# Kernel tuning notes

Measured on AMD Instinct MI355X. Metric: run time of the kernel, lower is better.

## Reference

```python
import jax, jax.numpy as jnp
import numpy as np

B, L, DIM, HEAD_DIM, COND = 16, 1025, 1024, 64, 256
N_HEADS = DIM // HEAD_DIM
EPS = 1e-6


def _make_cos_sin():
    # freqs: head_dim//8 log-spaced frequencies in [pi, 10*pi]
    freqs = np.exp(np.linspace(np.log(np.pi), np.log(10 * np.pi), HEAD_DIM // 8)).astype(np.float32)
    # axial positions on a 32x32 grid (cell centers in [-1, 1]), with a zero pos prepended
    g = np.linspace(-1.0, 1.0, 33, dtype=np.float32)
    g = (g[:-1] + g[1:]) / 2
    hh, ww = np.meshgrid(g, g, indexing='ij')
    pos = np.stack([hh.ravel(), ww.ravel()], axis=-1)          # [1024, 2]
    pos = np.concatenate([np.zeros((1, 2), np.float32), pos])  # [1025, 2]
    theta = np.concatenate([pos[:, 0:1] * freqs, pos[:, 1:2] * freqs], axis=-1)  # [L, head_dim//4]
    return jnp.asarray(np.cos(theta)), jnp.asarray(np.sin(theta))


def setup_inputs() -> dict:
    key = jax.random.key(0)
    kx, kc, kn, kq, ko = jax.random.split(key, 5)
    cos, sin = _make_cos_sin()
    return {
        'x': jax.random.normal(kx, (B, L, DIM), jnp.float32),
        'cond': jax.random.normal(kc, (B, COND), jnp.float32),
        'w_norm': jax.random.normal(kn, (DIM, COND), jnp.float32) * 0.02,   # AdaRMSNorm linear (zero-init in training; random here)
        'w_qkv': jax.random.normal(kq, (3 * DIM, DIM), jnp.float32) * 0.02,
        'w_out': jax.random.normal(ko, (DIM, DIM), jnp.float32) * 0.02,
        'cos': cos,  # [L, head_dim//4]
        'sin': sin,
    }


def _rope(t, cos, sin):
    # partial non-interleaved rotary: rotate first 2*cos.shape[-1] dims, leave the rest
    half = cos.shape[-1]                      # head_dim//4
    t1 = t[..., :half]
    t2 = t[..., half:2 * half]
    rest = t[..., 2 * half:]
    c = cos[None, :, None, :]                 # [1, L, 1, half]
    s = sin[None, :, None, :]
    return jnp.concatenate([t1 * c - t2 * s, t2 * c + t1 * s, rest], axis=-1)


def reference(x, cond, w_norm, w_qkv, w_out, cos, sin):
    skip = x
    # AdaRMSNorm: scale = cond-linear + 1, normalized by rms(x) in fp32
    scale = cond @ w_norm.T + 1.0                                    # [B, D]
    mean_sq = jnp.mean(jnp.square(x.astype(jnp.float32)), axis=-1, keepdims=True)
    xn = x * (scale[:, None, :] * jax.lax.rsqrt(mean_sq + EPS)).astype(x.dtype)
    # QKV projection
    qkv = (xn @ w_qkv.T).reshape(B, L, 3, N_HEADS, HEAD_DIM)
    q, k, v = qkv[:, :, 0], qkv[:, :, 1], qkv[:, :, 2]               # [B, L, H, hd]
    q = _rope(q, cos, sin)
    k = _rope(k, cos, sin)
    # causal attention (flash_attn default softmax scale = head_dim**-0.5)
    sm_scale = 1.0 / jnp.sqrt(jnp.asarray(HEAD_DIM, jnp.float32))
    scores = jnp.einsum('blhd,bmhd->bhlm', q, k) * sm_scale
    causal = jnp.tril(jnp.ones((L, L), bool))
    scores = jnp.where(causal[None, None], scores, jnp.finfo(scores.dtype).min)
    attn = jax.nn.softmax(scores, axis=-1)
    o = jnp.einsum('bhlm,bmhd->blhd', attn, v).reshape(B, L, DIM)
    return o @ w_out.T + skip
```

## Files before the change

kernel.cpp:

```cpp
#include <hip/hip_runtime.h>
#include <hip/hip_bf16.h>
#include <cstdint>

typedef __bf16 bf16;
typedef bf16 bf16x4 __attribute__((ext_vector_type(4)));
typedef bf16 bf16x8 __attribute__((ext_vector_type(8)));
typedef float f32x4 __attribute__((ext_vector_type(4)));
typedef float f32x16 __attribute__((ext_vector_type(16)));
typedef uint32_t u32x4 __attribute__((ext_vector_type(4)));

#define NB 16
#define NL 1025
#define NDIM 1024
#define NHEADS 16
#define NCOND 256
#define NBH (NB*NHEADS)
#define NML (NB*NL)
#define LP 1056
#define NSLOT 17
#define QSCALE (0.125f * 1.44269504088896340736f)

__device__ __forceinline__ void gload16(const void* g, void* l) {
  __builtin_amdgcn_global_load_lds(
      (const __attribute__((address_space(1))) void*)(uintptr_t)g,
      (__attribute__((address_space(3))) void*)(uintptr_t)l,
      16, 0, 0);
}

__device__ __forceinline__ float fexp2(float x) {
  return __builtin_amdgcn_exp2f(x);
}

__device__ __forceinline__ uint32_t cvtpk(float lo, float hi) {
  uint32_t r;
  asm("v_cvt_pk_bf16_f32 %0, %1, %2" : "=v"(r) : "v"(lo), "v"(hi));
  return r;
}

__device__ __forceinline__ f32x16 zero16() {
  f32x16 z;
#pragma unroll
  for (int i = 0; i < 16; ++i) z[i] = 0.f;
  return z;
}

__global__ __launch_bounds__(256) void k_scale(const float* __restrict__ cond,
                                               const float* __restrict__ wn,
                                               float* __restrict__ scl) {
  __shared__ float cs[NCOND];
  const int b = blockIdx.x, t = threadIdx.x;
  cs[t] = cond[b * NCOND + t];
  __syncthreads();
#pragma unroll
  for (int dd = 0; dd < 4; ++dd) {
    const int d = t * 4 + dd;
    const float4* w = (const float4*)(wn + (size_t)d * NCOND);
    float acc = 1.0f;
    for (int c4 = 0; c4 < NCOND / 4; ++c4) {
      float4 wv = w[c4];
      acc += wv.x * cs[c4*4] + wv.y * cs[c4*4+1] + wv.z * cs[c4*4+2] + wv.w * cs[c4*4+3];
    }
    scl[b * NDIM + d] = acc;
  }
}

__global__ __launch_bounds__(256) void k_cast(const float* __restrict__ src,
                                              bf16* __restrict__ dst, int n) {
  const int i = (blockIdx.x * 256 + threadIdx.x) * 4;
  if (i < n) {
    float4 v = *(const float4*)(src + i);
    bf16x4 o;
    o[0] = (bf16)v.x; o[1] = (bf16)v.y; o[2] = (bf16)v.z; o[3] = (bf16)v.w;
    *(bf16x4*)(dst + i) = o;
  }
}

__global__ __launch_bounds__(256) void k_rmsnorm(const float* __restrict__ x,
                                                 const float* __restrict__ scl,
                                                 bf16* __restrict__ xn) {
  const int row = blockIdx.x, t = threadIdx.x;
  const int b = row / NL;
  const float* xr = x + (size_t)row * NDIM;
  float4 v = *(const float4*)(xr + t * 4);
  float ss = v.x*v.x + v.y*v.y + v.z*v.z + v.w*v.w;
#pragma unroll
  for (int o = 1; o < 64; o <<= 1) ss += __shfl_xor(ss, o);
  __shared__ float red[4];
  if ((t & 63) == 0) red[t >> 6] = ss;
  __syncthreads();
  const float tot = red[0] + red[1] + red[2] + red[3];
  const float rn = rsqrtf(tot * (1.0f / NDIM) + 1e-6f);
  const float4 sc = *(const float4*)(scl + b * NDIM + t * 4);
  bf16x4 o4;
  o4[0] = (bf16)(v.x * sc.x * rn);
  o4[1] = (bf16)(v.y * sc.y * rn);
  o4[2] = (bf16)(v.z * sc.z * rn);
  o4[3] = (bf16)(v.w * sc.w * rn);
  *(bf16x4*)(xn + (size_t)row * NDIM + t * 4) = o4;
}

template <int EPI>
__global__ __launch_bounds__(256) void k_gemm(const bf16* __restrict__ A,
                                              const bf16* __restrict__ Bm,
                                              int M, int N, int K,
                                              float* __restrict__ Cf,
                                              const float* __restrict__ skip,
                                              bf16* __restrict__ qro,
                                              bf16* __restrict__ kro,
                                              bf16* __restrict__ vto,
                                              const float* __restrict__ cosT,
                                              const float* __restrict__ sinT) {
  __shared__ bf16 Als[2][128 * 64];
  __shared__ bf16 Bls[2][128 * 64];
  const int t = threadIdx.x;
  const int wave = t >> 6, lane = t & 63;
  const int g = lane >> 4, c = lane & 15;
  const int wm = wave >> 1, wn_ = wave & 1;

  const int nxb = N >> 7;
  const int nwg = gridDim.x;
  const int cpx = nwg >> 3;
  const int bid = blockIdx.x;
  const int swz = (nwg & 7) ? bid : (bid & 7) * cpx + (bid >> 3);
  const int m0 = (swz / nxb) * 128, n0 = (swz % nxb) * 128;
  const int NT = K >> 6;

  const int srow = lane >> 3;
  const int scol = ((lane & 7) ^ srow) * 8;

  f32x4 acc[4][4];
#pragma unroll
  for (int i = 0; i < 4; ++i)
#pragma unroll
    for (int j = 0; j < 4; ++j) acc[i][j] = f32x4{0.f, 0.f, 0.f, 0.f};

  auto stage = [&](int kt, int q) {
    const int k0 = kt << 6;
#pragma unroll
    for (int i = 0; i < 4; ++i) {
      const int seg = wave * 4 + i;
      int arow = m0 + seg * 8 + srow;
      if (arow >= M) arow = M - 1;
      gload16(A + (size_t)arow * K + k0 + scol, &Als[q][seg * 512]);
      const int brow = n0 + seg * 8 + srow;
      gload16(Bm + (size_t)brow * K + k0 + scol, &Bls[q][seg * 512]);
    }
  };

  stage(0, 0);
  for (int kt = 0; kt < NT; ++kt) {
    const int cur = kt & 1;
    if (kt + 1 < NT) {
      stage(kt + 1, cur ^ 1);
      asm volatile("s_waitcnt vmcnt(8)" ::: "memory");
    } else {
      asm volatile("s_waitcnt vmcnt(0)" ::: "memory");
    }
    __builtin_amdgcn_s_barrier();
    asm volatile("" ::: "memory");
#pragma unroll
    for (int kc = 0; kc < 2; ++kc) {
      bf16x8 af[4], bfr[4];
#pragma unroll
      for (int mi = 0; mi < 4; ++mi) {
        const int r = wm * 64 + mi * 16 + c;
        const int gg = ((kc * 4 + g) ^ (c & 7)) * 8;
        af[mi] = *(const bf16x8*)&Als[cur][r * 64 + gg];
      }
#pragma unroll
      for (int ni = 0; ni < 4; ++ni) {
        const int r = wn_ * 64 + ni * 16 + c;
        const int gg = ((kc * 4 + g) ^ (c & 7)) * 8;
        bfr[ni] = *(const bf16x8*)&Bls[cur][r * 64 + gg];
      }
      __builtin_amdgcn_s_setprio(1);
#pragma unroll
      for (int mi = 0; mi < 4; ++mi)
#pragma unroll
        for (int ni = 0; ni < 4; ++ni)
          acc[mi][ni] = __builtin_amdgcn_mfma_f32_16x16x32_bf16(af[mi], bfr[ni], acc[mi][ni], 0, 0, 0);
      __builtin_amdgcn_s_setprio(0);
    }
    asm volatile("" ::: "memory");
    __builtin_amdgcn_s_barrier();
  }

  if (EPI == 1) {
#pragma unroll
    for (int mi = 0; mi < 4; ++mi) {
      const int rb = m0 + wm * 64 + mi * 16 + g * 4;
#pragma unroll
      for (int ni = 0; ni < 4; ++ni) {
        const int col = n0 + wn_ * 64 + ni * 16 + c;
#pragma unroll
        for (int j = 0; j < 4; ++j) {
          const int row = rb + j;
          if (row < M) {
            const size_t idx = (size_t)row * N + col;
            Cf[idx] = acc[mi][ni][j] + skip[idx];
          }
        }
      }
    }
  } else {
    const int ncol0 = n0 + wn_ * 64;
    const int type = ncol0 >> 10;
    const int hd = (ncol0 & 1023) >> 6;
    if (type == 2) {
#pragma unroll
      for (int mi = 0; mi < 4; ++mi) {
        const int rb = m0 + wm * 64 + mi * 16 + g * 4;
        const int b0 = rb / NL, b3 = (rb + 3) / NL;
        if (rb + 3 < M && b0 == b3) {
          const int l0_ = rb - b0 * NL;
          const size_t bhb = (size_t)(b0 * NHEADS + hd) * 64;
#pragma unroll
          for (int ni = 0; ni < 4; ++ni) {
            const int d = ni * 16 + c;
            bf16x4 v4;
#pragma unroll
            for (int j = 0; j < 4; ++j) v4[j] = (bf16)acc[mi][ni][j];
            *(bf16x4*)(vto + (bhb + d) * LP + l0_) = v4;
          }
        } else {
#pragma unroll
          for (int j = 0; j < 4; ++j) {
            const int row = rb + j;
            if (row < M) {
              const int b_ = row / NL, l = row - b_ * NL;
              const size_t bhb = (size_t)(b_ * NHEADS + hd) * 64;
#pragma unroll
              for (int ni = 0; ni < 4; ++ni)
                vto[(bhb + ni * 16 + c) * LP + l] = (bf16)acc[mi][ni][j];
            }
          }
        }
      }
    } else {
      bf16* dst = (type == 0) ? qro : kro;
      const float qs = (type == 0) ? QSCALE : 1.0f;
#pragma unroll
      for (int mi = 0; mi < 4; ++mi) {
        const int rb = m0 + wm * 64 + mi * 16 + g * 4;
#pragma unroll
        for (int j = 0; j < 4; ++j) {
          const int row = rb + j;
          if (row < M) {
            const int b_ = row / NL, l = row - b_ * NL;
            const float cf = cosT[l * 16 + c], sf = sinT[l * 16 + c];
            const float a0 = acc[mi][0][j], a1 = acc[mi][1][j];
            const float r0 = (a0 * cf - a1 * sf) * qs;
            const float r1 = (a1 * cf + a0 * sf) * qs;
            const float r2 = acc[mi][2][j] * qs;
            const float r3 = acc[mi][3][j] * qs;
            const size_t bse = ((size_t)(b_ * NHEADS + hd) * NL + l) * 64;
            dst[bse + c]      = (bf16)r0;
            dst[bse + 16 + c] = (bf16)r1;
            dst[bse + 32 + c] = (bf16)r2;
            dst[bse + 48 + c] = (bf16)r3;
          }
        }
      }
    }
  }
}

__global__ __launch_bounds__(64) void k_attn(const bf16* __restrict__ qr,
                                             const bf16* __restrict__ kr,
                                             const bf16* __restrict__ vt,
                                             bf16* __restrict__ oa) {
  const int bid = blockIdx.x;
  const int lbid = (bid & 7) * (NBH * NSLOT / 8) + (bid >> 3);
  const int slot = lbid % NSLOT, bh = lbid / NSLOT;
  const int b = bh >> 4, h = bh & 15;
  const int lane = threadIdx.x;
  const int ql = lane & 31;
  const int hh = lane >> 5;
  const bf16* qb = qr + (size_t)bh * NL * 64;
  const bf16* kb = kr + (size_t)bh * NL * 64;
  const bf16* vb = vt + (size_t)bh * 64 * LP;

  auto run = [&](const int t) {
    const int q0 = t * 32;
    const int qabs = q0 + ql;
    const int qrow = (q0 + ql < NL) ? q0 + ql : NL - 1;
    bf16x8 bQ[4];
#pragma unroll
    for (int kc = 0; kc < 4; ++kc)
      bQ[kc] = *(const bf16x8*)(qb + (size_t)qrow * 64 + kc * 16 + hh * 8);

    f32x16 od0 = zero16(), od1 = zero16();
    float ls = 0.f;

    const int qmax = (q0 + 31 < NL - 1) ? q0 + 31 : NL - 1;
    const int nt = qmax / 64 + 1;

    bf16x8 aK[2][4];
    auto loadK = [&](int kv0) {
#pragma unroll
      for (int blk = 0; blk < 2; ++blk) {
        int r = kv0 + blk * 32 + ql; if (r >= NL) r = NL - 1;
        const bf16* kp = kb + (size_t)r * 64 + hh * 8;
#pragma unroll
        for (int kc = 0; kc < 4; ++kc)
          aK[blk][kc] = *(const bf16x8*)(kp + kc * 16);
      }
    };
    loadK(0);

    for (int tk = 0; tk < nt; ++tk) {
      const int kv0 = tk * 64;

      bf16x8 vf[2][4];
#pragma unroll
      for (int dblk = 0; dblk < 2; ++dblk) {
        const bf16* vp = vb + (size_t)(dblk * 32 + ql) * LP;
#pragma unroll
        for (int kc = 0; kc < 4; ++kc) {
          int col = kv0 + kc * 16 + hh * 8;
          if (col > LP - 8) col = LP - 8;
          vf[dblk][kc] = *(const bf16x8*)(vp + col);
        }
      }

      f32x16 s0 = zero16(), s1 = zero16();
#pragma unroll
      for (int kc = 0; kc < 4; ++kc)
        s0 = __builtin_amdgcn_mfma_f32_32x32x16_bf16(aK[0][kc], bQ[kc], s0, 0, 0, 0);
#pragma unroll
      for (int kc = 0; kc < 4; ++kc)
        s1 = __builtin_amdgcn_mfma_f32_32x32x16_bf16(aK[1][kc], bQ[kc], s1, 0, 0, 0);

      if (tk + 1 < nt) loadK(kv0 + 64);

      const bool needmask = (kv0 + 63 > q0);
      bf16x8 pa[4];
#pragma unroll
      for (int blk = 0; blk < 2; ++blk) {
        const f32x16& s = blk ? s1 : s0;
        float p[16];
#pragma unroll
        for (int r = 0; r < 16; ++r) {
          float v = s[r];
          if (needmask) {
            const int kvabs = kv0 + blk * 32 + (r & 3) + 8 * (r >> 2) + 4 * hh;
            if (kvabs > qabs) v = -1e30f;
          }
          p[r] = fexp2(v);
        }
        ls += (((p[0]+p[1])+(p[2]+p[3])) + ((p[4]+p[5])+(p[6]+p[7])))
            + (((p[8]+p[9])+(p[10]+p[11])) + ((p[12]+p[13])+(p[14]+p[15])));
        uint32_t w[8];
#pragma unroll
        for (int a = 0; a < 8; ++a) w[a] = cvtpk(p[2*a], p[2*a+1]);
        const uint32_t sel0 = hh ? w[0] : w[2];
        const uint32_t sel1 = hh ? w[1] : w[3];
        const uint32_t sel2 = hh ? w[4] : w[6];
        const uint32_t sel3 = hh ? w[5] : w[7];
        const uint32_t ex0 = (uint32_t)__shfl_xor((int)sel0, 32);
        const uint32_t ex1 = (uint32_t)__shfl_xor((int)sel1, 32);
        const uint32_t ex2 = (uint32_t)__shfl_xor((int)sel2, 32);
        const uint32_t ex3 = (uint32_t)__shfl_xor((int)sel3, 32);
        u32x4 w0_, w1_;
        w0_[0] = hh ? ex0 : w[0];
        w0_[1] = hh ? ex1 : w[1];
        w0_[2] = hh ? w[2] : ex0;
        w0_[3] = hh ? w[3] : ex1;
        w1_[0] = hh ? ex2 : w[4];
        w1_[1] = hh ? ex3 : w[5];
        w1_[2] = hh ? w[6] : ex2;
        w1_[3] = hh ? w[7] : ex3;
        pa[2*blk]     = __builtin_bit_cast(bf16x8, w0_);
        pa[2*blk + 1] = __builtin_bit_cast(bf16x8, w1_);
      }

#pragma unroll
      for (int kc = 0; kc < 4; ++kc) {
        od0 = __builtin_amdgcn_mfma_f32_32x32x16_bf16(pa[kc], vf[0][kc], od0, 0, 0, 0);
        od1 = __builtin_amdgcn_mfma_f32_32x32x16_bf16(pa[kc], vf[1][kc], od1, 0, 0, 0);
      }
    }

    const float tot = ls + __shfl_xor(ls, 32);
    const float invOwn = 1.0f / tot;
#pragma unroll
    for (int r = 0; r < 16; ++r) {
      const int qrl = (r & 3) + 8 * (r >> 2) + 4 * hh;
      const float inv = __shfl(invOwn, qrl);
      const int row = q0 + qrl;
      if (row < NL) {
        const size_t ob = (size_t)(b * NL + row) * NDIM + h * 64;
        oa[ob + ql]      = (bf16)(od0[r] * inv);
        oa[ob + 32 + ql] = (bf16)(od1[r] * inv);
      }
    }
  };

  if (slot < 16) { run(slot); run(31 - slot); }
  else           { run(32); }
}

extern "C" void kernel_launch(void* const* d_in, const int* in_sizes, int n_in,
                              void* d_out, int out_size, void* d_ws, size_t ws_size,
                              hipStream_t stream) {
  const float* x     = (const float*)d_in[0];
  const float* cond  = (const float*)d_in[1];
  const float* wnorm = (const float*)d_in[2];
  const float* wqkv  = (const float*)d_in[3];
  const float* wout  = (const float*)d_in[4];
  const float* cosT  = (const float*)d_in[5];
  const float* sinT  = (const float*)d_in[6];
  float* out = (float*)d_out;
  char* ws = (char*)d_ws;

  float* s_scl = (float*)(ws);
  bf16*  s_wq  = (bf16*)(ws + 65536);
  bf16*  s_wo  = (bf16*)(ws + 6356992);
  bf16*  s_xn  = (bf16*)(ws + 8454144);
  bf16*  s_qr  = (bf16*)(ws + 142802944);
  bf16*  s_kr  = (bf16*)(ws + 176390144);
  bf16*  s_vt  = (bf16*)(ws + 209977344);

  k_scale<<<NB, 256, 0, stream>>>(cond, wnorm, s_scl);
  k_cast<<<3072, 256, 0, stream>>>(wqkv, s_wq, 3 * NDIM * NDIM);
  k_cast<<<1024, 256, 0, stream>>>(wout, s_wo, NDIM * NDIM);
  k_rmsnorm<<<NML, 256, 0, stream>>>(x, s_scl, s_xn);
  k_gemm<2><<<3096, 256, 0, stream>>>(s_xn, s_wq, NML, 3 * NDIM, NDIM,
                                      nullptr, nullptr, s_qr, s_kr, s_vt,
                                      cosT, sinT);
  k_attn<<<NBH * NSLOT, 64, 0, stream>>>(s_qr, s_kr, s_vt, s_xn);
  k_gemm<1><<<1032, 256, 0, stream>>>(s_xn, s_wo, NML, NDIM, NDIM,
                                      out, x, nullptr, nullptr, nullptr,
                                      nullptr, nullptr);
}
```

Measured before the change: 434.0 us.

## Fuse paired query tiles into one KV loop sharing K/V loads

The attention block used to process its two query tiles one after the other, reloading K and V for each. It now walks the KV sequence once and feeds each K/V tile to both query tiles, so the shorter tile A shares loads with tile B. This halves K/V global traffic for paired slots and interleaves independent MFMA/softmax chains to hide latency. In exchange it doubles live accumulators and query registers, which may raise register pressure and lower occupancy.

```diff
diff --git a/kernel.cpp b/kernel.cpp
--- a/kernel.cpp
+++ b/kernel.cpp
@@ -280,107 +280,145 @@
   const bf16* kb = kr + (size_t)bh * NL * 64;
   const bf16* vb = vt + (size_t)bh * 64 * LP;
 
-  auto run = [&](const int t) {
-    const int q0 = t * 32;
-    const int qabs = q0 + ql;
-    const int qrow = (q0 + ql < NL) ? q0 + ql : NL - 1;
-    bf16x8 bQ[4];
+  const int tA = (slot < 16) ? slot : -1;
+  const int tB = (slot < 16) ? 31 - slot : 32;
+  const bool hasA = (tA >= 0);
+
+  const int q0A = tA * 32, q0B = tB * 32;
+  const int qabsA = q0A + ql, qabsB = q0B + ql;
+
+  bf16x8 bQA[4], bQB[4];
+  {
+    const int qrB = (q0B + ql < NL) ? q0B + ql : NL - 1;
 #pragma unroll
     for (int kc = 0; kc < 4; ++kc)
-      bQ[kc] = *(const bf16x8*)(qb + (size_t)qrow * 64 + kc * 16 + hh * 8);
-
-    f32x16 od0 = zero16(), od1 = zero16();
-    float ls = 0.f;
-
-    const int qmax = (q0 + 31 < NL - 1) ? q0 + 31 : NL - 1;
-    const int nt = qmax / 64 + 1;
-
-    bf16x8 aK[2][4];
-    auto loadK = [&](int kv0) {
-#pragma unroll
-      for (int blk = 0; blk < 2; ++blk) {
-        int r = kv0 + blk * 32 + ql; if (r >= NL) r = NL - 1;
-        const bf16* kp = kb + (size_t)r * 64 + hh * 8;
-#pragma unroll
-        for (int kc = 0; kc < 4; ++kc)
-          aK[blk][kc] = *(const bf16x8*)(kp + kc * 16);
-      }
-    };
-    loadK(0);
-
-    for (int tk = 0; tk < nt; ++tk) {
-      const int kv0 = tk * 64;
-
-      bf16x8 vf[2][4];
-#pragma unroll
-      for (int dblk = 0; dblk < 2; ++dblk) {
-        const bf16* vp = vb + (size_t)(dblk * 32 + ql) * LP;
-#pragma unroll
-        for (int kc = 0; kc < 4; ++kc) {
-          int col = kv0 + kc * 16 + hh * 8;
-          if (col > LP - 8) col = LP - 8;
-          vf[dblk][kc] = *(const bf16x8*)(vp + col);
+      bQB[kc] = *(const bf16x8*)(qb + (size_t)qrB * 64 + kc * 16 + hh * 8);
+    const int qrA = hasA ? q0A + ql : 0;
+#pragma unroll
+    for (int kc = 0; kc < 4; ++kc)
+      bQA[kc] = *(const bf16x8*)(qb + (size_t)qrA * 64 + kc * 16 + hh * 8);
+  }
+
+  f32x16 odA0 = zero16(), odA1 = zero16(), odB0 = zero16(), odB1 = zero16();
+  float lsA = 0.f, lsB = 0.f;
+
+  const int ntA = hasA ? ((q0A + 31) / 64 + 1) : 0;
+  const int qmaxB = (q0B + 31 < NL - 1) ? q0B + 31 : NL - 1;
+  const int ntB = qmaxB / 64 + 1;
+
+  bf16x8 aK[2][4];
+  auto loadK = [&](int kv0) {
+#pragma unroll
+    for (int blk = 0; blk < 2; ++blk) {
+      int r = kv0 + blk * 32 + ql; if (r >= NL) r = NL - 1;
+      const bf16* kp = kb + (size_t)r * 64 + hh * 8;
+#pragma unroll
+      for (int kc = 0; kc < 4; ++kc)
+        aK[blk][kc] = *(const bf16x8*)(kp + kc * 16);
+    }
+  };
+  loadK(0);
+
+  auto smrepack = [&](const f32x16& s0, const f32x16& s1, int kv0, int q0,
+                      int qabs, float& ls, bf16x8 (&pa)[4]) {
+    const bool needmask = (kv0 + 63 > q0);
+#pragma unroll
+    for (int blk = 0; blk < 2; ++blk) {
+      const f32x16& s = blk ? s1 : s0;
+      float p[16];
+#pragma unroll
+      for (int r = 0; r < 16; ++r) {
+        float v = s[r];
+        if (needmask) {
+          const int kvabs = kv0 + blk * 32 + (r & 3) + 8 * (r >> 2) + 4 * hh;
+          if (kvabs > qabs) v = -1e30f;
         }
-      }
-
+        p[r] = fexp2(v);
+      }
+      ls += (((p[0]+p[1])+(p[2]+p[3])) + ((p[4]+p[5])+(p[6]+p[7])))
+          + (((p[8]+p[9])+(p[10]+p[11])) + ((p[12]+p[13])+(p[14]+p[15])));
+      uint32_t w[8];
+#pragma unroll
+      for (int a = 0; a < 8; ++a) w[a] = cvtpk(p[2*a], p[2*a+1]);
+      const uint32_t sel0 = hh ? w[0] : w[2];
+      const uint32_t sel1 = hh ? w[1] : w[3];
+      const uint32_t sel2 = hh ? w[4] : w[6];
+      const uint32_t sel3 = hh ? w[5] : w[7];
+      const uint32_t ex0 = (uint32_t)__shfl_xor((int)sel0, 32);
+      const uint32_t ex1 = (uint32_t)__shfl_xor((int)sel1, 32);
+      const uint32_t ex2 = (uint32_t)__shfl_xor((int)sel2, 32);
+      const uint32_t ex3 = (uint32_t)__shfl_xor((int)sel3, 32);
+      u32x4 w0_, w1_;
+      w0_[0] = hh ? ex0 : w[0];
+      w0_[1] = hh ? ex1 : w[1];
+      w0_[2] = hh ? w[2] : ex0;
+      w0_[3] = hh ? w[3] : ex1;
+      w1_[0] = hh ? ex2 : w[4];
+      w1_[1] = hh ? ex3 : w[5];
+      w1_[2] = hh ? w[6] : ex2;
+      w1_[3] = hh ? w[7] : ex3;
+      pa[2*blk]     = __builtin_bit_cast(bf16x8, w0_);
+      pa[2*blk + 1] = __builtin_bit_cast(bf16x8, w1_);
+    }
+  };
+
+  for (int tk = 0; tk < ntB; ++tk) {
+    const int kv0 = tk * 64;
+    const bool actA = hasA && (tk < ntA);
+
+    bf16x8 vf[2][4];
+#pragma unroll
+    for (int dblk = 0; dblk < 2; ++dblk) {
+      const bf16* vp = vb + (size_t)(dblk * 32 + ql) * LP;
+#pragma unroll
+      for (int kc = 0; kc < 4; ++kc) {
+        int col = kv0 + kc * 16 + hh * 8;
+        if (col > LP - 8) col = LP - 8;
+        vf[dblk][kc] = *(const bf16x8*)(vp + col);
+      }
+    }
+
+    bf16x8 paA[4];
+    if (actA) {
       f32x16 s0 = zero16(), s1 = zero16();
 #pragma unroll
       for (int kc = 0; kc < 4; ++kc)
-        s0 = __builtin_amdgcn_mfma_f32_32x32x16_bf16(aK[0][kc], bQ[kc], s0, 0, 0, 0);
+        s0 = __builtin_amdgcn_mfma_f32_32x32x16_bf16(aK[0][kc], bQA[kc], s0, 0, 0, 0);
 #pragma unroll
       for (int kc = 0; kc < 4; ++kc)
-        s1 = __builtin_amdgcn_mfma_f32_32x32x16_bf16(aK[1][kc], bQ[kc], s1, 0, 0, 0);
-
-      if (tk + 1 < nt) loadK(kv0 + 64);
-
-      const bool needmask = (kv0 + 63 > q0);
-      bf16x8 pa[4];
-#pragma unroll
-      for (int blk = 0; blk < 2; ++blk) {
-        const f32x16& s = blk ? s1 : s0;
-        float p[16];
-#pragma unroll
-        for (int r = 0; r < 16; ++r) {
-          float v = s[r];
-          if (needmask) {
-            const int kvabs = kv0 + blk * 32 + (r & 3) + 8 * (r >> 2) + 4 * hh;
-            if (kvabs > qabs) v = -1e30f;
-          }
-          p[r] = fexp2(v);
-        }
-        ls += (((p[0]+p[1])+(p[2]+p[3])) + ((p[4]+p[5])+(p[6]+p[7])))
-            + (((p[8]+p[9])+(p[10]+p[11])) + ((p[12]+p[13])+(p[14]+p[15])));
-        uint32_t w[8];
-#pragma unroll
-        for (int a = 0; a < 8; ++a) w[a] = cvtpk(p[2*a], p[2*a+1]);
-        const uint32_t sel0 = hh ? w[0] : w[2];
-        const uint32_t sel1 = hh ? w[1] : w[3];
-        const uint32_t sel2 = hh ? w[4] : w[6];
-        const uint32_t sel3 = hh ? w[5] : w[7];
-        const uint32_t ex0 = (uint32_t)__shfl_xor((int)sel0, 32);
-        const uint32_t ex1 = (uint32_t)__shfl_xor((int)sel1, 32);
-        const uint32_t ex2 = (uint32_t)__shfl_xor((int)sel2, 32);
-        const uint32_t ex3 = (uint32_t)__shfl_xor((int)sel3, 32);
-        u32x4 w0_, w1_;
-        w0_[0] = hh ? ex0 : w[0];
-        w0_[1] = hh ? ex1 : w[1];
-        w0_[2] = hh ? w[2] : ex0;
-        w0_[3] = hh ? w[3] : ex1;
-        w1_[0] = hh ? ex2 : w[4];
-        w1_[1] = hh ? ex3 : w[5];
-        w1_[2] = hh ? w[6] : ex2;
-        w1_[3] = hh ? w[7] : ex3;
-        pa[2*blk]     = __builtin_bit_cast(bf16x8, w0_);
-        pa[2*blk + 1] = __builtin_bit_cast(bf16x8, w1_);
-      }
-
+        s1 = __builtin_amdgcn_mfma_f32_32x32x16_bf16(aK[1][kc], bQA[kc], s1, 0, 0, 0);
+      smrepack(s0, s1, kv0, q0A, qabsA, lsA, paA);
+    }
+
+    f32x16 sB0 = zero16(), sB1 = zero16();
+#pragma unroll
+    for (int kc = 0; kc < 4; ++kc)
+      sB0 = __builtin_amdgcn_mfma_f32_32x32x16_bf16(aK[0][kc], bQB[kc], sB0, 0, 0, 0);
+#pragma unroll
+    for (int kc = 0; kc < 4; ++kc)
+      sB1 = __builtin_amdgcn_mfma_f32_32x32x16_bf16(aK[1][kc], bQB[kc], sB1, 0, 0, 0);
+
+    if (tk + 1 < ntB) loadK(kv0 + 64);
+
+    if (actA) {
 #pragma unroll
       for (int kc = 0; kc < 4; ++kc) {
-        od0 = __builtin_amdgcn_mfma_f32_32x32x16_bf16(pa[kc], vf[0][kc], od0, 0, 0, 0);
-        od1 = __builtin_amdgcn_mfma_f32_32x32x16_bf16(pa[kc], vf[1][kc], od1, 0, 0, 0);
-      }
-    }
-
+        odA0 = __builtin_amdgcn_mfma_f32_32x32x16_bf16(paA[kc], vf[0][kc], odA0, 0, 0, 0);
+        odA1 = __builtin_amdgcn_mfma_f32_32x32x16_bf16(paA[kc], vf[1][kc], odA1, 0, 0, 0);
+      }
+    }
+
+    bf16x8 paB[4];
+    smrepack(sB0, sB1, kv0, q0B, qabsB, lsB, paB);
+
+#pragma unroll
+    for (int kc = 0; kc < 4; ++kc) {
+      odB0 = __builtin_amdgcn_mfma_f32_32x32x16_bf16(paB[kc], vf[0][kc], odB0, 0, 0, 0);
+      odB1 = __builtin_amdgcn_mfma_f32_32x32x16_bf16(paB[kc], vf[1][kc], odB1, 0, 0, 0);
+    }
+  }
+
+  auto fin = [&](int q0, float ls, const f32x16& od0, const f32x16& od1) {
     const float tot = ls + __shfl_xor(ls, 32);
     const float invOwn = 1.0f / tot;
 #pragma unroll
@@ -395,9 +433,8 @@
       }
     }
   };
-
-  if (slot < 16) { run(slot); run(31 - slot); }
-  else           { run(32); }
+  if (hasA) fin(q0A, lsA, odA0, odA1);
+  fin(q0B, lsB, odB0, odB1);
 }
 
 extern "C" void kernel_launch(void* const* d_in, const int* in_sizes, int n_in,
```

Result: no change. 427.9 us (-1.4%).
